# Kernel tuning notes

Measured on AMD Instinct MI355X. Metric: run time of the kernel, lower is better.

Reference implementation:

```python
import jax, jax.numpy as jnp
import numpy as np

NEG_SLOPE = 0.2  # PyG GATConv default negative_slope
EPS = 1e-16     # PyG softmax denominator epsilon


def gat_layer(x, src, dst, W, att_src, att_dst, bias, N):
    """PyG-style GATConv: gather -> leaky-relu score -> segment softmax -> scatter-add.
    x: [N, F_in], W: [F_in, H*C], att_src/att_dst: [H, C], bias: [H*C].
    src/dst: [E] edge endpoints (messages flow src -> dst), self-loops included.
    """
    H, C = att_src.shape
    h = (x @ W).reshape(N, H, C)                       # [N, H, C]
    a_s = jnp.sum(h * att_src, axis=-1)                # [N, H]
    a_d = jnp.sum(h * att_dst, axis=-1)                # [N, H]
    e = a_s[src] + a_d[dst]                            # [E, H]
    e = jnp.where(e > 0, e, NEG_SLOPE * e)             # leaky relu
    m = jax.ops.segment_max(e, dst, num_segments=N)    # [N, H] (self-loops ensure every node hit)
    p = jnp.exp(e - m[dst])                            # [E, H]
    s = jax.ops.segment_sum(p, dst, num_segments=N)    # [N, H]
    alpha = p / (s[dst] + EPS)                         # [E, H]
    out = jax.ops.segment_sum(alpha[:, :, None] * h[src], dst, num_segments=N)  # [N, H, C]
    return out.reshape(N, H * C) + bias


def setup_inputs() -> dict:
    key = jax.random.key(0)
    ks = jax.random.split(key, 12)
    N, E = 100000, 1600000
    x = jax.random.normal(ks[0], (N, 1), dtype=jnp.float32)
    edge_index = jax.random.randint(ks[1], (2, E), 0, N, dtype=jnp.int32)
    sc = 0.1
    # conv1: in=1, heads=4, out=8
    W1 = jax.random.normal(ks[2], (1, 32), dtype=jnp.float32) * sc
    att_src1 = jax.random.normal(ks[3], (4, 8), dtype=jnp.float32) * sc
    att_dst1 = jax.random.normal(ks[4], (4, 8), dtype=jnp.float32) * sc
    bias1 = jnp.zeros((32,), dtype=jnp.float32)
    # conv2: in=32, heads=8, out=8
    W2 = jax.random.normal(ks[5], (32, 64), dtype=jnp.float32) * sc
    att_src2 = jax.random.normal(ks[6], (8, 8), dtype=jnp.float32) * sc
    att_dst2 = jax.random.normal(ks[7], (8, 8), dtype=jnp.float32) * sc
    bias2 = jnp.zeros((64,), dtype=jnp.float32)
    # fc2: 64 -> 1
    fc_w = jax.random.normal(ks[8], (64, 1), dtype=jnp.float32) * sc
    fc_b = jnp.zeros((1,), dtype=jnp.float32)
    return {"x": x, "edge_index": edge_index,
            "W1": W1, "att_src1": att_src1, "att_dst1": att_dst1, "bias1": bias1,
            "W2": W2, "att_src2": att_src2, "att_dst2": att_dst2, "bias2": bias2,
            "fc_w": fc_w, "fc_b": fc_b}


def reference(x, edge_index, W1, att_src1, att_dst1, bias1,
              W2, att_src2, att_dst2, bias2, fc_w, fc_b):
    N = x.shape[0]
    loop = jnp.arange(N, dtype=edge_index.dtype)       # add_self_loops=True (PyG default)
    src = jnp.concatenate([edge_index[0], loop])
    dst = jnp.concatenate([edge_index[1], loop])
    h = jax.nn.elu(gat_layer(x, src, dst, W1, att_src1, att_dst1, bias1, N))
    h = jax.nn.elu(gat_layer(h, src, dst, W2, att_src2, att_dst2, bias2, N))
    return h @ fc_w + fc_b                             # [N, 1]
```

## Files before the change

### kernel.cpp

```cpp
#include <hip/hip_runtime.h>
#include <hip/hip_fp16.h>
#include <cmath>

#define TPB 256
#define NSLOPE 0.2f
#define SEPS 1e-16f

#define BSH 7
#define BNODES 128
#define NBMAX 1024
#define NCHUNK 512
#define SCTPB 1024
#define SCSTAGE 3360
#define STAGE 2816
#define MAXDEG 96

__device__ __forceinline__ float lrelu(float v) { return v > 0.f ? v : NSLOPE * v; }
__device__ __forceinline__ float elu1(float v)  { return v > 0.f ? v : expm1f(v); }
__device__ __forceinline__ float elu1f(float v) { return v > 0.f ? v : __expf(v) - 1.f; }

__global__ void k_prep(const float* __restrict__ W1, const float* __restrict__ as1,
                       const float* __restrict__ ad1, float* __restrict__ SD,
                       unsigned* __restrict__ bucketCursor, int NB, unsigned cap) {
    int t = threadIdx.x;
    for (int i = t; i < NB; i += blockDim.x) bucketCursor[(size_t)i * 16] = (unsigned)i * cap;
    if (t < 8) {
        int h = t & 3;
        const float* att = (t >= 4) ? ad1 : as1;
        float acc = 0.f;
        #pragma unroll
        for (int c = 0; c < 8; ++c) acc += W1[h*8+c] * att[h*8+c];
        SD[t] = acc;
    }
}

__global__ void k_bscatter(const int* __restrict__ srcI, const int* __restrict__ dstI,
                           int E, int N, int NB, int chunk,
                           unsigned* __restrict__ bucketCursor, int* __restrict__ pk) {
    __shared__ int cnt[NBMAX];
    __shared__ unsigned base[NBMAX];
    __shared__ int offl[NBMAX];
    __shared__ int rval[SCSTAGE];
    __shared__ unsigned short rbkt[SCSTAGE];
    int t = threadIdx.x;
    int ET = E + N;
    int beg = blockIdx.x * chunk;
    int end = min(beg + chunk, ET);
    int m = end - beg;
    for (int i = t; i < NBMAX; i += blockDim.x) cnt[i] = 0;
    __syncthreads();
    for (int e = beg + t; e < end; e += blockDim.x) {
        int d = (e < E) ? dstI[e] : (e - E);
        atomicAdd(&cnt[d >> BSH], 1);
    }
    __syncthreads();
    int v = (t < NBMAX) ? cnt[t] : 0;
    if (t < NBMAX) base[t] = (unsigned)v;
    __syncthreads();
    for (int off = 1; off < NBMAX; off <<= 1) {
        unsigned u = (t >= off && t < NBMAX) ? base[t - off] : 0u;
        __syncthreads();
        if (t < NBMAX) base[t] += u;
        __syncthreads();
    }
    if (t < NBMAX) offl[t] = (int)base[t] - v;
    __syncthreads();
    if (t < NB) {
        base[t] = v ? atomicAdd(&bucketCursor[(size_t)t * 16], (unsigned)v) : 0u;
        cnt[t] = 0;
    }
    __syncthreads();
    if (m <= SCSTAGE) {
        for (int e = beg + t; e < end; e += blockDim.x) {
            int s, d;
            if (e < E) { s = srcI[e]; d = dstI[e]; } else { s = d = e - E; }
            int b = d >> BSH;
            int r = atomicAdd(&cnt[b], 1);
            int slot = offl[b] + r;
            rval[slot] = (s << BSH) | (d & (BNODES - 1));
            rbkt[slot] = (unsigned short)b;
        }
        __syncthreads();
        for (int slot = t; slot < m; slot += blockDim.x) {
            int b = rbkt[slot];
            pk[base[b] + (unsigned)(slot - offl[b])] = rval[slot];
        }
    } else {
        for (int e = beg + t; e < end; e += blockDim.x) {
            int s, d;
            if (e < E) { s = srcI[e]; d = dstI[e]; } else { s = d = e - E; }
            int b = d >> BSH;
            int r = atomicAdd(&cnt[b], 1);
            pk[base[b] + (unsigned)r] = (s << BSH) | (d & (BNODES - 1));
        }
    }
}

__global__ void k_mega(const int* __restrict__ pk, const unsigned* __restrict__ bucketCursor,
                       unsigned cap,
                       const float* __restrict__ x, const float* __restrict__ SD,
                       const float* __restrict__ W1, const float* __restrict__ b1,
                       const float* __restrict__ W2, const float* __restrict__ attS,
                       const float* __restrict__ attD, int N,
                       unsigned* __restrict__ offsets, int* __restrict__ sortedSrc,
                       __half* __restrict__ h2h, float* __restrict__ aS, float* __restrict__ aD) {
    __shared__ int stage[STAGE];
    __shared__ int sorted[STAGE];
    __shared__ int cnt[BNODES];
    __shared__ int offl[BNODES];
    __shared__ float lds1[BNODES][36];
    int b = blockIdx.x, t = threadIdx.x;
    unsigned rbeg = (unsigned)b * cap;
    int m = (int)(bucketCursor[(size_t)b * 16] - rbeg);
    bool inLds = (m <= STAGE);
    if (t < BNODES) cnt[t] = 0;
    __syncthreads();
    if (inLds) {
        for (int i = t; i < m; i += TPB) stage[i] = pk[rbeg + i];
        __syncthreads();
        for (int i = t; i < m; i += TPB) atomicAdd(&cnt[stage[i] & (BNODES - 1)], 1);
    } else {
        for (int i = t; i < m; i += TPB) atomicAdd(&cnt[pk[rbeg + i] & (BNODES - 1)], 1);
    }
    __syncthreads();
    int v = (t < BNODES) ? cnt[t] : 0;
    if (t < BNODES) offl[t] = v;
    __syncthreads();
    for (int off = 1; off < BNODES; off <<= 1) {
        int u = (t >= off && t < BNODES) ? offl[t - off] : 0;
        __syncthreads();
        if (t < BNODES) offl[t] += u;
        __syncthreads();
    }
    if (t < BNODES) {
        int ex = offl[t] - v;
        int d = (b << BSH) + t;
        if (d < N) offsets[d] = ((rbeg + (unsigned)ex) << 10) | (unsigned)v;
        cnt[t] = 0;
        offl[t] = ex;
    }
    __syncthreads();
    if (inLds) {
        for (int i = t; i < m; i += TPB) {
            int p = stage[i];
            int dl = p & (BNODES - 1);
            int r = atomicAdd(&cnt[dl], 1);
            sorted[offl[dl] + r] = p >> BSH;
        }
        __syncthreads();
        for (int i = t; i < m; i += TPB) sortedSrc[rbeg + i] = sorted[i];
    } else {
        for (int i = t; i < m; i += TPB) {
            int p = pk[rbeg + i];
            int dl = p & (BNODES - 1);
            int r = atomicAdd(&cnt[dl], 1);
            sortedSrc[rbeg + (unsigned)(offl[dl] + r)] = p >> BSH;
        }
        __syncthreads();
    }
    __syncthreads();
    int n = t >> 1, half = t & 1;
    int base2 = b << BSH;
    int d2 = base2 + n;
    bool active = (d2 < N);
    float s0 = 0.f, s1 = 0.f, s2 = 0.f, s3 = 0.f;
    float g0 = 0.f, g1 = 0.f, g2 = 0.f, g3 = 0.f;
    if (active) {
        int deg = cnt[n];
        int lbeg = offl[n];
        float xd = x[d2];
        float S0 = SD[0], S1 = SD[1], S2 = SD[2], S3 = SD[3];
        float D0 = xd*SD[4], D1 = xd*SD[5], D2 = xd*SD[6], D3 = xd*SD[7];
        int dh = (deg + 1) >> 1;
        int i0 = lbeg + (half ? dh : 0);
        int rem = half ? (deg - dh) : dh;
        int i = i0;
        for (; rem >= 2; rem -= 2, i += 2) {
            int a0 = inLds ? sorted[i]   : sortedSrc[rbeg + i];
            int a1 = inLds ? sorted[i+1] : sortedSrc[rbeg + i + 1];
            float x0 = x[a0], x1 = x[a1];
            float p;
            p = __expf(lrelu(x0*S0 + D0)); s0 += p; g0 += p * x0;
            p = __expf(lrelu(x0*S1 + D1)); s1 += p; g1 += p * x0;
            p = __expf(lrelu(x0*S2 + D2)); s2 += p; g2 += p * x0;
            p = __expf(lrelu(x0*S3 + D3)); s3 += p; g3 += p * x0;
            p = __expf(lrelu(x1*S0 + D0)); s0 += p; g0 += p * x1;
            p = __expf(lrelu(x1*S1 + D1)); s1 += p; g1 += p * x1;
            p = __expf(lrelu(x1*S2 + D2)); s2 += p; g2 += p * x1;
            p = __expf(lrelu(x1*S3 + D3)); s3 += p; g3 += p * x1;
        }
        if (rem > 0) {
            int a0 = inLds ? sorted[i] : sortedSrc[rbeg + i];
            float xs = x[a0];
            float p;
            p = __expf(lrelu(xs*S0 + D0)); s0 += p; g0 += p * xs;
            p = __expf(lrelu(xs*S1 + D1)); s1 += p; g1 += p * xs;
            p = __expf(lrelu(xs*S2 + D2)); s2 += p; g2 += p * xs;
            p = __expf(lrelu(xs*S3 + D3)); s3 += p; g3 += p * xs;
        }
    }
    s0 += __shfl_xor(s0, 1); s1 += __shfl_xor(s1, 1);
    s2 += __shfl_xor(s2, 1); s3 += __shfl_xor(s3, 1);
    g0 += __shfl_xor(g0, 1); g1 += __shfl_xor(g1, 1);
    g2 += __shfl_xor(g2, 1); g3 += __shfl_xor(g3, 1);
    if (active) {
        float gg[4];
        gg[0] = g0 / (s0 + SEPS); gg[1] = g1 / (s1 + SEPS);
        gg[2] = g2 / (s2 + SEPS); gg[3] = g3 / (s3 + SEPS);
        int h0 = half * 2;
        #pragma unroll
        for (int hh = 0; hh < 2; ++hh)
            #pragma unroll
            for (int cc = 0; cc < 8; ++cc)
                lds1[n][(h0+hh)*8+cc] = elu1(gg[h0+hh] * W1[(h0+hh)*8+cc] + b1[(h0+hh)*8+cc]);
    }
    __syncthreads();
    int lane = t & 63;
    int sub = t >> 6;
    float w2r[32];
    #pragma unroll
    for (int k = 0; k < 32; ++k) w2r[k] = W2[k*64 + lane];
    float attSl = attS[lane], attDl = attD[lane];
    int nCnt = min(BNODES, N - base2);
    for (int nn = sub; nn < nCnt; nn += 4) {
        const float4* row4 = (const float4*)lds1[nn];
        float acc = 0.f;
        #pragma unroll
        for (int k4 = 0; k4 < 8; ++k4) {
            float4 rv = row4[k4];
            acc += rv.x*w2r[4*k4] + rv.y*w2r[4*k4+1] + rv.z*w2r[4*k4+2] + rv.w*w2r[4*k4+3];
        }
        int node = base2 + nn;
        h2h[(size_t)node*64 + lane] = __float2half(acc);
        float ps = acc * attSl;
        float pd = acc * attDl;
        #pragma unroll
        for (int mm = 1; mm < 8; mm <<= 1) {
            ps += __shfl_xor(ps, mm);
            pd += __shfl_xor(pd, mm);
        }
        int hh = lane >> 3, cc = lane & 7;
        if (cc == 0) aS[(size_t)node*8 + hh] = ps;
        if (cc == 1) aD[(size_t)node*8 + hh] = pd;
    }
}

__global__ void k_agg(const unsigned* __restrict__ offsets, const int* __restrict__ ss,
                      const float* __restrict__ aS, const float* __restrict__ aD,
                      const __half* __restrict__ h2h, const float* __restrict__ b2,
                      const float* __restrict__ fcw, const float* __restrict__ fcb,
                      float* __restrict__ out, int N) {
    __shared__ float pl[4][MAXDEG * 8];
    __shared__ int   sl[4][MAXDEG];
    int lane = threadIdx.x & 63;
    int w = threadIdx.x >> 6;
    int d = blockIdx.x * 4 + w;
    if (d >= N) return;
    unsigned u = offsets[d];
    unsigned beg = u >> 10;
    int deg = (int)(u & 1023u);
    int lH   = lane & 31;
    int half = lane >> 5;
    int hh   = lH >> 2;
    float sum = 0.f, ax = 0.f, ay = 0.f;
    if (deg <= MAXDEG) {
        for (int j = lane; j < deg; j += 64) sl[w][j] = ss[beg + j];
        float adp = aD[(size_t)d*8 + (lane & 7)];
        int tot = deg * 8;
        for (int base = 0; base < tot; base += 64) {
            int idx = base + lane;
            if (idx < tot) {
                int s = sl[w][idx >> 3];
                pl[w][idx] = __expf(lrelu(aS[(size_t)s*8 + (lane & 7)] + adp));
            }
        }
        int e = 0;
        for (; e + 8 <= deg; e += 8) {
            int e0 = e + half, e1 = e + 2 + half, e2 = e + 4 + half, e3 = e + 6 + half;
            int s0 = sl[w][e0], s1 = sl[w][e1], s2 = sl[w][e2], s3 = sl[w][e3];
            float p0 = pl[w][e0*8 + hh], p1 = pl[w][e1*8 + hh];
            float p2 = pl[w][e2*8 + hh], p3 = pl[w][e3*8 + hh];
            float2 g0 = __half22float2(*(const __half2*)(h2h + (size_t)s0*64 + 2*lH));
            float2 g1 = __half22float2(*(const __half2*)(h2h + (size_t)s1*64 + 2*lH));
            float2 g2 = __half22float2(*(const __half2*)(h2h + (size_t)s2*64 + 2*lH));
            float2 g3 = __half22float2(*(const __half2*)(h2h + (size_t)s3*64 + 2*lH));
            ax += p0*g0.x + p1*g1.x + p2*g2.x + p3*g3.x;
            ay += p0*g0.y + p1*g1.y + p2*g2.y + p3*g3.y;
            sum += (p0 + p1) + (p2 + p3);
        }
        for (; e + 2 <= deg; e += 2) {
            int e0 = e + half;
            int s0 = sl[w][e0];
            float p0 = pl[w][e0*8 + hh];
            float2 g0 = __half22float2(*(const __half2*)(h2h + (size_t)s0*64 + 2*lH));
            ax += p0*g0.x; ay += p0*g0.y; sum += p0;
        }
        if (e < deg) {
            int s0 = sl[w][e];
            float p0 = (half == 0) ? pl[w][e*8 + hh] : 0.f;
            float2 g0 = __half22float2(*(const __half2*)(h2h + (size_t)s0*64 + 2*lH));
            ax += p0*g0.x; ay += p0*g0.y; sum += p0;
        }
    } else {
        float adh = aD[(size_t)d*8 + hh];
        for (int e = half; e < deg; e += 2) {
            int s = ss[beg + e];
            float p = __expf(lrelu(aS[(size_t)s*8 + hh] + adh));
            float2 g = __half22float2(*(const __half2*)(h2h + (size_t)s*64 + 2*lH));
            ax += p*g.x; ay += p*g.y; sum += p;
        }
    }
    ax  += __shfl_xor(ax, 32);
    ay  += __shfl_xor(ay, 32);
    sum += __shfl_xor(sum, 32);
    float inv = 1.f / (sum + SEPS);
    float tt = elu1f(ax*inv + b2[2*lH]) * fcw[2*lH]
             + elu1f(ay*inv + b2[2*lH+1]) * fcw[2*lH+1];
    #pragma unroll
    for (int m = 16; m; m >>= 1) tt += __shfl_xor(tt, m);
    if (lane == 0) out[d] = tt + fcb[0];
}

extern "C" void kernel_launch(void* const* d_in, const int* in_sizes, int n_in,
                              void* d_out, int out_size, void* d_ws, size_t ws_size,
                              hipStream_t stream) {
    const float* x    = (const float*)d_in[0];
    const int*   ei   = (const int*)  d_in[1];
    const float* W1   = (const float*)d_in[2];
    const float* as1  = (const float*)d_in[3];
    const float* ad1  = (const float*)d_in[4];
    const float* b1   = (const float*)d_in[5];
    const float* W2   = (const float*)d_in[6];
    const float* attS2= (const float*)d_in[7];
    const float* attD2= (const float*)d_in[8];
    const float* b2   = (const float*)d_in[9];
    const float* fcw  = (const float*)d_in[10];
    const float* fcb  = (const float*)d_in[11];
    float* out = (float*)d_out;

    int N = in_sizes[0];
    int E = in_sizes[1] / 2;
    int ET = E + N;
    int NB = (N + BNODES - 1) / BNODES;
    unsigned cap = (unsigned)((ET + NB - 1) / NB + 512);
    cap = (cap + 3u) & ~3u;
    size_t padded = (size_t)NB * cap;

    const int* srcI = ei;
    const int* dstI = ei + E;

    float* ws = (float*)d_ws;
    size_t off = 0;
    float*    SD           = ws + off; off += 16;
    unsigned* bucketCursor = (unsigned*)(ws + off); off += (size_t)NBMAX * 16;
    unsigned* offsets      = (unsigned*)(ws + off); off += (size_t)N + 16;
    int*      pk           = (int*)(ws + off); off += padded;
    int*      sortedSrc    = (int*)(ws + off); off += padded;
    float*    aS2          = ws + off; off += (size_t)N * 8;
    float*    aD2          = ws + off; off += (size_t)N * 8;
    __half*   h2h          = (__half*)(ws + off); off += (size_t)N * 32;

    k_prep<<<1, 1024, 0, stream>>>(W1, as1, ad1, SD, bucketCursor, NB, cap);

    int chunk = (ET + NCHUNK - 1) / NCHUNK;
    k_bscatter<<<NCHUNK, SCTPB, 0, stream>>>(srcI, dstI, E, N, NB, chunk, bucketCursor, pk);
    k_mega    <<<NB, TPB, 0, stream>>>(pk, bucketCursor, cap, x, SD, W1, b1, W2, attS2, attD2,
                                       N, offsets, sortedSrc, h2h, aS2, aD2);
    k_agg     <<<(N + 3) / 4, TPB, 0, stream>>>(offsets, sortedSrc, aS2, aD2, h2h,
                                                b2, fcw, fcb, out, N);
}
```

Measured before the change: 229.0 us.

## Fuse all stages into one cooperative persistent kernel with grid syncs

Replaces the four separate launches (prep, bucket scatter, per-bucket sort plus layer 1, layer-2 aggregation) with one cooperative kernel of 256 blocks of 1024 threads, separated by grid.sync barriers. Bucket offsets are no longer claimed with global atomics. Per-block counts are written to a matrix and prefix-summed deterministically per bucket, and the LDS staging path of the scatter is dropped. Blocks loop over buckets and destination nodes in a persistent style, and layer 1 now uses 8 lanes per node. This aims to cut launch gaps and atomic contention, at the cost of only 256 blocks of parallelism and the overhead of the grid barriers.

Result: slower. 457.1 us (+99.6%).

```diff
diff --git a/kernel.cpp b/kernel.cpp
--- a/kernel.cpp
+++ b/kernel.cpp
@@ -1,17 +1,18 @@
 #include <hip/hip_runtime.h>
+#include <hip/hip_cooperative_groups.h>
 #include <hip/hip_fp16.h>
 #include <cmath>
 
-#define TPB 256
+namespace cg = cooperative_groups;
+
 #define NSLOPE 0.2f
 #define SEPS 1e-16f
 
 #define BSH 7
 #define BNODES 128
 #define NBMAX 1024
-#define NCHUNK 512
-#define SCTPB 1024
-#define SCSTAGE 3360
+#define NBLK 256
+#define NTHR 1024
 #define STAGE 2816
 #define MAXDEG 96
 
@@ -19,12 +20,47 @@
 __device__ __forceinline__ float elu1(float v)  { return v > 0.f ? v : expm1f(v); }
 __device__ __forceinline__ float elu1f(float v) { return v > 0.f ? v : __expf(v) - 1.f; }
 
-__global__ void k_prep(const float* __restrict__ W1, const float* __restrict__ as1,
-                       const float* __restrict__ ad1, float* __restrict__ SD,
-                       unsigned* __restrict__ bucketCursor, int NB, unsigned cap) {
-    int t = threadIdx.x;
-    for (int i = t; i < NB; i += blockDim.x) bucketCursor[(size_t)i * 16] = (unsigned)i * cap;
-    if (t < 8) {
+struct P02s { int cnt[NBMAX]; unsigned basel[NBMAX]; };
+struct P3s  { int stage[STAGE]; int sorted[STAGE]; int cnt[BNODES]; int offl[BNODES];
+              float lds1[BNODES][36]; };
+struct P4s  { float pl[16][MAXDEG * 8]; int sl[16][MAXDEG]; };
+union SmemU { P02s a; P3s b; P4s c; };
+
+__global__ __launch_bounds__(NTHR, 4)
+void k_fused(const int* __restrict__ ei, const float* __restrict__ x,
+             const float* __restrict__ W1, const float* __restrict__ as1,
+             const float* __restrict__ ad1, const float* __restrict__ b1,
+             const float* __restrict__ W2, const float* __restrict__ attS,
+             const float* __restrict__ attD, const float* __restrict__ b2,
+             const float* __restrict__ fcw, const float* __restrict__ fcb,
+             float* __restrict__ out, float* __restrict__ ws, int E, int N) {
+    __shared__ SmemU sm;
+    cg::grid_group grid = cg::this_grid();
+    int t = threadIdx.x, blk = blockIdx.x;
+    int ET = E + N;
+    int NB = (N + BNODES - 1) >> BSH;
+    unsigned cap = (unsigned)((ET + NB - 1) / NB + 512);
+    cap = (cap + 3u) & ~3u;
+    size_t padded = (size_t)NB * cap;
+
+    const int* srcI = ei;
+    const int* dstI = ei + E;
+
+    float*    SD        = ws;
+    int*      blkCnt    = (int*)(ws + 16);
+    int*      bucketLen = blkCnt + (size_t)NBMAX * NBLK;
+    unsigned* offsets   = (unsigned*)(bucketLen + NBMAX);
+    int*      pk        = (int*)(offsets + (size_t)N + 16);
+    int*      sortedSrc = pk + padded;
+    float*    aS        = (float*)(sortedSrc + padded);
+    float*    aD        = aS + (size_t)N * 8;
+    __half*   h2h       = (__half*)(aD + (size_t)N * 8);
+
+    int chunk = (ET + NBLK - 1) / NBLK;
+    int cbeg = blk * chunk;
+    int cend = min(cbeg + chunk, ET);
+
+    if (blk == 0 && t < 8) {
         int h = t & 3;
         const float* att = (t >= 4) ? ad1 : as1;
         float acc = 0.f;
@@ -32,293 +68,238 @@
         for (int c = 0; c < 8; ++c) acc += W1[h*8+c] * att[h*8+c];
         SD[t] = acc;
     }
-}
-
-__global__ void k_bscatter(const int* __restrict__ srcI, const int* __restrict__ dstI,
-                           int E, int N, int NB, int chunk,
-                           unsigned* __restrict__ bucketCursor, int* __restrict__ pk) {
-    __shared__ int cnt[NBMAX];
-    __shared__ unsigned base[NBMAX];
-    __shared__ int offl[NBMAX];
-    __shared__ int rval[SCSTAGE];
-    __shared__ unsigned short rbkt[SCSTAGE];
-    int t = threadIdx.x;
-    int ET = E + N;
-    int beg = blockIdx.x * chunk;
-    int end = min(beg + chunk, ET);
-    int m = end - beg;
-    for (int i = t; i < NBMAX; i += blockDim.x) cnt[i] = 0;
+    for (int i = t; i < NB; i += NTHR) sm.a.cnt[i] = 0;
     __syncthreads();
-    for (int e = beg + t; e < end; e += blockDim.x) {
+    for (int e = cbeg + t; e < cend; e += NTHR) {
         int d = (e < E) ? dstI[e] : (e - E);
-        atomicAdd(&cnt[d >> BSH], 1);
+        atomicAdd(&sm.a.cnt[d >> BSH], 1);
     }
     __syncthreads();
-    int v = (t < NBMAX) ? cnt[t] : 0;
-    if (t < NBMAX) base[t] = (unsigned)v;
+    for (int j = t; j < NB; j += NTHR) blkCnt[(size_t)j * NBLK + blk] = sm.a.cnt[j];
+    grid.sync();
+
+    {
+        int tid = blk * NTHR + t;
+        if (tid < NB) {
+            unsigned run = (unsigned)tid * cap;
+            size_t rowb = (size_t)tid * NBLK;
+            for (int b = 0; b < NBLK; ++b) {
+                int c = blkCnt[rowb + b];
+                blkCnt[rowb + b] = (int)run;
+                run += (unsigned)c;
+            }
+            bucketLen[tid] = (int)(run - (unsigned)tid * cap);
+        }
+    }
+    grid.sync();
+
+    for (int j = t; j < NB; j += NTHR) {
+        sm.a.basel[j] = (unsigned)blkCnt[(size_t)j * NBLK + blk];
+        sm.a.cnt[j] = 0;
+    }
     __syncthreads();
-    for (int off = 1; off < NBMAX; off <<= 1) {
-        unsigned u = (t >= off && t < NBMAX) ? base[t - off] : 0u;
-        __syncthreads();
-        if (t < NBMAX) base[t] += u;
-        __syncthreads();
-    }
-    if (t < NBMAX) offl[t] = (int)base[t] - v;
-    __syncthreads();
-    if (t < NB) {
-        base[t] = v ? atomicAdd(&bucketCursor[(size_t)t * 16], (unsigned)v) : 0u;
-        cnt[t] = 0;
-    }
-    __syncthreads();
-    if (m <= SCSTAGE) {
-        for (int e = beg + t; e < end; e += blockDim.x) {
-            int s, d;
-            if (e < E) { s = srcI[e]; d = dstI[e]; } else { s = d = e - E; }
-            int b = d >> BSH;
-            int r = atomicAdd(&cnt[b], 1);
-            int slot = offl[b] + r;
-            rval[slot] = (s << BSH) | (d & (BNODES - 1));
-            rbkt[slot] = (unsigned short)b;
-        }
-        __syncthreads();
-        for (int slot = t; slot < m; slot += blockDim.x) {
-            int b = rbkt[slot];
-            pk[base[b] + (unsigned)(slot - offl[b])] = rval[slot];
-        }
-    } else {
-        for (int e = beg + t; e < end; e += blockDim.x) {
-            int s, d;
-            if (e < E) { s = srcI[e]; d = dstI[e]; } else { s = d = e - E; }
-            int b = d >> BSH;
-            int r = atomicAdd(&cnt[b], 1);
-            pk[base[b] + (unsigned)r] = (s << BSH) | (d & (BNODES - 1));
-        }
-    }
-}
-
-__global__ void k_mega(const int* __restrict__ pk, const unsigned* __restrict__ bucketCursor,
-                       unsigned cap,
-                       const float* __restrict__ x, const float* __restrict__ SD,
-                       const float* __restrict__ W1, const float* __restrict__ b1,
-                       const float* __restrict__ W2, const float* __restrict__ attS,
-                       const float* __restrict__ attD, int N,
-                       unsigned* __restrict__ offsets, int* __restrict__ sortedSrc,
-                       __half* __restrict__ h2h, float* __restrict__ aS, float* __restrict__ aD) {
-    __shared__ int stage[STAGE];
-    __shared__ int sorted[STAGE];
-    __shared__ int cnt[BNODES];
-    __shared__ int offl[BNODES];
-    __shared__ float lds1[BNODES][36];
-    int b = blockIdx.x, t = threadIdx.x;
-    unsigned rbeg = (unsigned)b * cap;
-    int m = (int)(bucketCursor[(size_t)b * 16] - rbeg);
-    bool inLds = (m <= STAGE);
-    if (t < BNODES) cnt[t] = 0;
-    __syncthreads();
-    if (inLds) {
-        for (int i = t; i < m; i += TPB) stage[i] = pk[rbeg + i];
-        __syncthreads();
-        for (int i = t; i < m; i += TPB) atomicAdd(&cnt[stage[i] & (BNODES - 1)], 1);
-    } else {
-        for (int i = t; i < m; i += TPB) atomicAdd(&cnt[pk[rbeg + i] & (BNODES - 1)], 1);
-    }
-    __syncthreads();
-    int v = (t < BNODES) ? cnt[t] : 0;
-    if (t < BNODES) offl[t] = v;
-    __syncthreads();
-    for (int off = 1; off < BNODES; off <<= 1) {
-        int u = (t >= off && t < BNODES) ? offl[t - off] : 0;
-        __syncthreads();
-        if (t < BNODES) offl[t] += u;
-        __syncthreads();
-    }
-    if (t < BNODES) {
-        int ex = offl[t] - v;
-        int d = (b << BSH) + t;
-        if (d < N) offsets[d] = ((rbeg + (unsigned)ex) << 10) | (unsigned)v;
-        cnt[t] = 0;
-        offl[t] = ex;
-    }
-    __syncthreads();
-    if (inLds) {
-        for (int i = t; i < m; i += TPB) {
-            int p = stage[i];
-            int dl = p & (BNODES - 1);
-            int r = atomicAdd(&cnt[dl], 1);
-            sorted[offl[dl] + r] = p >> BSH;
-        }
-        __syncthreads();
-        for (int i = t; i < m; i += TPB) sortedSrc[rbeg + i] = sorted[i];
-    } else {
-        for (int i = t; i < m; i += TPB) {
-            int p = pk[rbeg + i];
-            int dl = p & (BNODES - 1);
-            int r = atomicAdd(&cnt[dl], 1);
-            sortedSrc[rbeg + (unsigned)(offl[dl] + r)] = p >> BSH;
-        }
-        __syncthreads();
-    }
-    __syncthreads();
-    int n = t >> 1, half = t & 1;
-    int base2 = b << BSH;
-    int d2 = base2 + n;
-    bool active = (d2 < N);
-    float s0 = 0.f, s1 = 0.f, s2 = 0.f, s3 = 0.f;
-    float g0 = 0.f, g1 = 0.f, g2 = 0.f, g3 = 0.f;
-    if (active) {
-        int deg = cnt[n];
-        int lbeg = offl[n];
-        float xd = x[d2];
-        float S0 = SD[0], S1 = SD[1], S2 = SD[2], S3 = SD[3];
-        float D0 = xd*SD[4], D1 = xd*SD[5], D2 = xd*SD[6], D3 = xd*SD[7];
-        int dh = (deg + 1) >> 1;
-        int i0 = lbeg + (half ? dh : 0);
-        int rem = half ? (deg - dh) : dh;
-        int i = i0;
-        for (; rem >= 2; rem -= 2, i += 2) {
-            int a0 = inLds ? sorted[i]   : sortedSrc[rbeg + i];
-            int a1 = inLds ? sorted[i+1] : sortedSrc[rbeg + i + 1];
-            float x0 = x[a0], x1 = x[a1];
-            float p;
-            p = __expf(lrelu(x0*S0 + D0)); s0 += p; g0 += p * x0;
-            p = __expf(lrelu(x0*S1 + D1)); s1 += p; g1 += p * x0;
-            p = __expf(lrelu(x0*S2 + D2)); s2 += p; g2 += p * x0;
-            p = __expf(lrelu(x0*S3 + D3)); s3 += p; g3 += p * x0;
-            p = __expf(lrelu(x1*S0 + D0)); s0 += p; g0 += p * x1;
-            p = __expf(lrelu(x1*S1 + D1)); s1 += p; g1 += p * x1;
-            p = __expf(lrelu(x1*S2 + D2)); s2 += p; g2 += p * x1;
-            p = __expf(lrelu(x1*S3 + D3)); s3 += p; g3 += p * x1;
-        }
-        if (rem > 0) {
-            int a0 = inLds ? sorted[i] : sortedSrc[rbeg + i];
-            float xs = x[a0];
-            float p;
-            p = __expf(lrelu(xs*S0 + D0)); s0 += p; g0 += p * xs;
-            p = __expf(lrelu(xs*S1 + D1)); s1 += p; g1 += p * xs;
-            p = __expf(lrelu(xs*S2 + D2)); s2 += p; g2 += p * xs;
-            p = __expf(lrelu(xs*S3 + D3)); s3 += p; g3 += p * xs;
-        }
-    }
-    s0 += __shfl_xor(s0, 1); s1 += __shfl_xor(s1, 1);
-    s2 += __shfl_xor(s2, 1); s3 += __shfl_xor(s3, 1);
-    g0 += __shfl_xor(g0, 1); g1 += __shfl_xor(g1, 1);
-    g2 += __shfl_xor(g2, 1); g3 += __shfl_xor(g3, 1);
-    if (active) {
-        float gg[4];
-        gg[0] = g0 / (s0 + SEPS); gg[1] = g1 / (s1 + SEPS);
-        gg[2] = g2 / (s2 + SEPS); gg[3] = g3 / (s3 + SEPS);
-        int h0 = half * 2;
-        #pragma unroll
-        for (int hh = 0; hh < 2; ++hh)
-            #pragma unroll
-            for (int cc = 0; cc < 8; ++cc)
-                lds1[n][(h0+hh)*8+cc] = elu1(gg[h0+hh] * W1[(h0+hh)*8+cc] + b1[(h0+hh)*8+cc]);
-    }
-    __syncthreads();
+    for (int e = cbeg + t; e < cend; e += NTHR) {
+        int s, d;
+        if (e < E) { s = srcI[e]; d = dstI[e]; } else { s = d = e - E; }
+        int j = d >> BSH;
+        int r = atomicAdd(&sm.a.cnt[j], 1);
+        pk[sm.a.basel[j] + (unsigned)r] = (s << BSH) | (d & (BNODES - 1));
+    }
+    grid.sync();
+
+    float S0 = SD[0], S1 = SD[1], S2 = SD[2], S3 = SD[3];
+    float SD4 = SD[4], SD5 = SD[5], SD6 = SD[6], SD7 = SD[7];
     int lane = t & 63;
-    int sub = t >> 6;
+    int wv = t >> 6;
     float w2r[32];
     #pragma unroll
     for (int k = 0; k < 32; ++k) w2r[k] = W2[k*64 + lane];
     float attSl = attS[lane], attDl = attD[lane];
-    int nCnt = min(BNODES, N - base2);
-    for (int nn = sub; nn < nCnt; nn += 4) {
-        const float4* row4 = (const float4*)lds1[nn];
-        float acc = 0.f;
-        #pragma unroll
-        for (int k4 = 0; k4 < 8; ++k4) {
-            float4 rv = row4[k4];
-            acc += rv.x*w2r[4*k4] + rv.y*w2r[4*k4+1] + rv.z*w2r[4*k4+2] + rv.w*w2r[4*k4+3];
-        }
-        int node = base2 + nn;
-        h2h[(size_t)node*64 + lane] = __float2half(acc);
-        float ps = acc * attSl;
-        float pd = acc * attDl;
-        #pragma unroll
-        for (int mm = 1; mm < 8; mm <<= 1) {
-            ps += __shfl_xor(ps, mm);
-            pd += __shfl_xor(pd, mm);
-        }
-        int hh = lane >> 3, cc = lane & 7;
-        if (cc == 0) aS[(size_t)node*8 + hh] = ps;
-        if (cc == 1) aD[(size_t)node*8 + hh] = pd;
-    }
-}
-
-__global__ void k_agg(const unsigned* __restrict__ offsets, const int* __restrict__ ss,
-                      const float* __restrict__ aS, const float* __restrict__ aD,
-                      const __half* __restrict__ h2h, const float* __restrict__ b2,
-                      const float* __restrict__ fcw, const float* __restrict__ fcb,
-                      float* __restrict__ out, int N) {
-    __shared__ float pl[4][MAXDEG * 8];
-    __shared__ int   sl[4][MAXDEG];
-    int lane = threadIdx.x & 63;
-    int w = threadIdx.x >> 6;
-    int d = blockIdx.x * 4 + w;
-    if (d >= N) return;
-    unsigned u = offsets[d];
-    unsigned beg = u >> 10;
-    int deg = (int)(u & 1023u);
-    int lH   = lane & 31;
-    int half = lane >> 5;
-    int hh   = lH >> 2;
-    float sum = 0.f, ax = 0.f, ay = 0.f;
-    if (deg <= MAXDEG) {
-        for (int j = lane; j < deg; j += 64) sl[w][j] = ss[beg + j];
-        float adp = aD[(size_t)d*8 + (lane & 7)];
-        int tot = deg * 8;
-        for (int base = 0; base < tot; base += 64) {
-            int idx = base + lane;
-            if (idx < tot) {
-                int s = sl[w][idx >> 3];
-                pl[w][idx] = __expf(lrelu(aS[(size_t)s*8 + (lane & 7)] + adp));
-            }
-        }
-        int e = 0;
-        for (; e + 8 <= deg; e += 8) {
-            int e0 = e + half, e1 = e + 2 + half, e2 = e + 4 + half, e3 = e + 6 + half;
-            int s0 = sl[w][e0], s1 = sl[w][e1], s2 = sl[w][e2], s3 = sl[w][e3];
-            float p0 = pl[w][e0*8 + hh], p1 = pl[w][e1*8 + hh];
-            float p2 = pl[w][e2*8 + hh], p3 = pl[w][e3*8 + hh];
-            float2 g0 = __half22float2(*(const __half2*)(h2h + (size_t)s0*64 + 2*lH));
-            float2 g1 = __half22float2(*(const __half2*)(h2h + (size_t)s1*64 + 2*lH));
-            float2 g2 = __half22float2(*(const __half2*)(h2h + (size_t)s2*64 + 2*lH));
-            float2 g3 = __half22float2(*(const __half2*)(h2h + (size_t)s3*64 + 2*lH));
-            ax += p0*g0.x + p1*g1.x + p2*g2.x + p3*g3.x;
-            ay += p0*g0.y + p1*g1.y + p2*g2.y + p3*g3.y;
-            sum += (p0 + p1) + (p2 + p3);
-        }
-        for (; e + 2 <= deg; e += 2) {
-            int e0 = e + half;
-            int s0 = sl[w][e0];
-            float p0 = pl[w][e0*8 + hh];
-            float2 g0 = __half22float2(*(const __half2*)(h2h + (size_t)s0*64 + 2*lH));
-            ax += p0*g0.x; ay += p0*g0.y; sum += p0;
-        }
-        if (e < deg) {
-            int s0 = sl[w][e];
-            float p0 = (half == 0) ? pl[w][e*8 + hh] : 0.f;
-            float2 g0 = __half22float2(*(const __half2*)(h2h + (size_t)s0*64 + 2*lH));
-            ax += p0*g0.x; ay += p0*g0.y; sum += p0;
-        }
-    } else {
-        float adh = aD[(size_t)d*8 + hh];
-        for (int e = half; e < deg; e += 2) {
-            int s = ss[beg + e];
-            float p = __expf(lrelu(aS[(size_t)s*8 + hh] + adh));
-            float2 g = __half22float2(*(const __half2*)(h2h + (size_t)s*64 + 2*lH));
-            ax += p*g.x; ay += p*g.y; sum += p;
-        }
-    }
-    ax  += __shfl_xor(ax, 32);
-    ay  += __shfl_xor(ay, 32);
-    sum += __shfl_xor(sum, 32);
-    float inv = 1.f / (sum + SEPS);
-    float tt = elu1f(ax*inv + b2[2*lH]) * fcw[2*lH]
-             + elu1f(ay*inv + b2[2*lH+1]) * fcw[2*lH+1];
-    #pragma unroll
-    for (int m = 16; m; m >>= 1) tt += __shfl_xor(tt, m);
-    if (lane == 0) out[d] = tt + fcb[0];
+    for (int b = blk; b < NB; b += NBLK) {
+        unsigned rbeg = (unsigned)b * cap;
+        int m = bucketLen[b];
+        bool inLds = (m <= STAGE);
+        __syncthreads();
+        if (t < BNODES) sm.b.cnt[t] = 0;
+        __syncthreads();
+        if (inLds) {
+            for (int i = t; i < m; i += NTHR) sm.b.stage[i] = pk[rbeg + i];
+            __syncthreads();
+            for (int i = t; i < m; i += NTHR) atomicAdd(&sm.b.cnt[sm.b.stage[i] & (BNODES-1)], 1);
+        } else {
+            for (int i = t; i < m; i += NTHR) atomicAdd(&sm.b.cnt[pk[rbeg + i] & (BNODES-1)], 1);
+        }
+        __syncthreads();
+        int v = (t < BNODES) ? sm.b.cnt[t] : 0;
+        if (t < BNODES) sm.b.offl[t] = v;
+        __syncthreads();
+        for (int off = 1; off < BNODES; off <<= 1) {
+            int u = (t >= off && t < BNODES) ? sm.b.offl[t - off] : 0;
+            __syncthreads();
+            if (t < BNODES) sm.b.offl[t] += u;
+            __syncthreads();
+        }
+        if (t < BNODES) {
+            int ex = sm.b.offl[t] - v;
+            int d = (b << BSH) + t;
+            if (d < N) offsets[d] = ((rbeg + (unsigned)ex) << 10) | (unsigned)v;
+            sm.b.cnt[t] = 0;
+            sm.b.offl[t] = ex;
+        }
+        __syncthreads();
+        if (inLds) {
+            for (int i = t; i < m; i += NTHR) {
+                int p = sm.b.stage[i];
+                int dl = p & (BNODES - 1);
+                int r = atomicAdd(&sm.b.cnt[dl], 1);
+                sm.b.sorted[sm.b.offl[dl] + r] = p >> BSH;
+            }
+            __syncthreads();
+            for (int i = t; i < m; i += NTHR) sortedSrc[rbeg + i] = sm.b.sorted[i];
+        } else {
+            for (int i = t; i < m; i += NTHR) {
+                int p = pk[rbeg + i];
+                int dl = p & (BNODES - 1);
+                int r = atomicAdd(&sm.b.cnt[dl], 1);
+                sortedSrc[rbeg + (unsigned)(sm.b.offl[dl] + r)] = p >> BSH;
+            }
+            __syncthreads();
+        }
+        __syncthreads();
+        int n = t >> 3, oct = t & 7;
+        int d2 = (b << BSH) + n;
+        bool active = (d2 < N);
+        float s0 = 0.f, s1 = 0.f, s2 = 0.f, s3 = 0.f;
+        float g0 = 0.f, g1 = 0.f, g2 = 0.f, g3 = 0.f;
+        if (active) {
+            int deg = sm.b.cnt[n];
+            int lbeg = sm.b.offl[n];
+            float xd = x[d2];
+            float D0 = xd*SD4, D1 = xd*SD5, D2 = xd*SD6, D3 = xd*SD7;
+            for (int i = lbeg + oct; i < lbeg + deg; i += 8) {
+                int a0 = inLds ? sm.b.sorted[i] : sortedSrc[rbeg + i];
+                float xs = x[a0];
+                float p;
+                p = __expf(lrelu(xs*S0 + D0)); s0 += p; g0 += p * xs;
+                p = __expf(lrelu(xs*S1 + D1)); s1 += p; g1 += p * xs;
+                p = __expf(lrelu(xs*S2 + D2)); s2 += p; g2 += p * xs;
+                p = __expf(lrelu(xs*S3 + D3)); s3 += p; g3 += p * xs;
+            }
+        }
+        s0 += __shfl_xor(s0, 1); s0 += __shfl_xor(s0, 2); s0 += __shfl_xor(s0, 4);
+        s1 += __shfl_xor(s1, 1); s1 += __shfl_xor(s1, 2); s1 += __shfl_xor(s1, 4);
+        s2 += __shfl_xor(s2, 1); s2 += __shfl_xor(s2, 2); s2 += __shfl_xor(s2, 4);
+        s3 += __shfl_xor(s3, 1); s3 += __shfl_xor(s3, 2); s3 += __shfl_xor(s3, 4);
+        g0 += __shfl_xor(g0, 1); g0 += __shfl_xor(g0, 2); g0 += __shfl_xor(g0, 4);
+        g1 += __shfl_xor(g1, 1); g1 += __shfl_xor(g1, 2); g1 += __shfl_xor(g1, 4);
+        g2 += __shfl_xor(g2, 1); g2 += __shfl_xor(g2, 2); g2 += __shfl_xor(g2, 4);
+        g3 += __shfl_xor(g3, 1); g3 += __shfl_xor(g3, 2); g3 += __shfl_xor(g3, 4);
+        if (active) {
+            int h = oct >> 1, c0 = (oct & 1) * 4;
+            float sq = (h == 0) ? s0 : (h == 1) ? s1 : (h == 2) ? s2 : s3;
+            float gq = (h == 0) ? g0 : (h == 1) ? g1 : (h == 2) ? g2 : g3;
+            float gg = gq / (sq + SEPS);
+            #pragma unroll
+            for (int cc = 0; cc < 4; ++cc)
+                sm.b.lds1[n][h*8 + c0 + cc] =
+                    elu1(gg * W1[h*8 + c0 + cc] + b1[h*8 + c0 + cc]);
+        }
+        __syncthreads();
+        int base2 = b << BSH;
+        int nCnt = min(BNODES, N - base2);
+        for (int nn = wv; nn < nCnt; nn += 16) {
+            const float4* row4 = (const float4*)sm.b.lds1[nn];
+            float acc = 0.f;
+            #pragma unroll
+            for (int k4 = 0; k4 < 8; ++k4) {
+                float4 rv = row4[k4];
+                acc += rv.x*w2r[4*k4] + rv.y*w2r[4*k4+1] + rv.z*w2r[4*k4+2] + rv.w*w2r[4*k4+3];
+            }
+            int node = base2 + nn;
+            h2h[(size_t)node*64 + lane] = __float2half(acc);
+            float ps = acc * attSl;
+            float pd = acc * attDl;
+            #pragma unroll
+            for (int mm = 1; mm < 8; mm <<= 1) {
+                ps += __shfl_xor(ps, mm);
+                pd += __shfl_xor(pd, mm);
+            }
+            int hh = lane >> 3, cc = lane & 7;
+            if (cc == 0) aS[(size_t)node*8 + hh] = ps;
+            if (cc == 1) aD[(size_t)node*8 + hh] = pd;
+        }
+    }
+    grid.sync();
+
+    {
+        float* plw = sm.c.pl[wv];
+        int*   slw = sm.c.sl[wv];
+        int lH   = lane & 31;
+        int half = lane >> 5;
+        int hh   = lH >> 2;
+        for (int d = blk * 16 + wv; d < N; d += NBLK * 16) {
+            unsigned u = offsets[d];
+            unsigned beg = u >> 10;
+            int deg = (int)(u & 1023u);
+            float sum = 0.f, ax = 0.f, ay = 0.f;
+            if (deg <= MAXDEG) {
+                for (int j = lane; j < deg; j += 64) slw[j] = sortedSrc[beg + j];
+                float adp = aD[(size_t)d*8 + (lane & 7)];
+                int tot = deg * 8;
+                for (int base = 0; base < tot; base += 64) {
+                    int idx = base + lane;
+                    if (idx < tot) {
+                        int s = slw[idx >> 3];
+                        plw[idx] = __expf(lrelu(aS[(size_t)s*8 + (lane & 7)] + adp));
+                    }
+                }
+                int e = 0;
+                for (; e + 8 <= deg; e += 8) {
+                    int e0 = e + half, e1 = e + 2 + half, e2 = e + 4 + half, e3 = e + 6 + half;
+                    int s0 = slw[e0], s1 = slw[e1], s2 = slw[e2], s3 = slw[e3];
+                    float p0 = plw[e0*8 + hh], p1 = plw[e1*8 + hh];
+                    float p2 = plw[e2*8 + hh], p3 = plw[e3*8 + hh];
+                    float2 g0 = __half22float2(*(const __half2*)(h2h + (size_t)s0*64 + 2*lH));
+                    float2 g1 = __half22float2(*(const __half2*)(h2h + (size_t)s1*64 + 2*lH));
+                    float2 g2 = __half22float2(*(const __half2*)(h2h + (size_t)s2*64 + 2*lH));
+                    float2 g3 = __half22float2(*(const __half2*)(h2h + (size_t)s3*64 + 2*lH));
+                    ax += p0*g0.x + p1*g1.x + p2*g2.x + p3*g3.x;
+                    ay += p0*g0.y + p1*g1.y + p2*g2.y + p3*g3.y;
+                    sum += (p0 + p1) + (p2 + p3);
+                }
+                for (; e + 2 <= deg; e += 2) {
+                    int e0 = e + half;
+                    int s0 = slw[e0];
+                    float p0 = plw[e0*8 + hh];
+                    float2 g0 = __half22float2(*(const __half2*)(h2h + (size_t)s0*64 + 2*lH));
+                    ax += p0*g0.x; ay += p0*g0.y; sum += p0;
+                }
+                if (e < deg) {
+                    int s0 = slw[e];
+                    float p0 = (half == 0) ? plw[e*8 + hh] : 0.f;
+                    float2 g0 = __half22float2(*(const __half2*)(h2h + (size_t)s0*64 + 2*lH));
+                    ax += p0*g0.x; ay += p0*g0.y; sum += p0;
+                }
+            } else {
+                float adh = aD[(size_t)d*8 + hh];
+                for (int e = half; e < deg; e += 2) {
+                    int s = sortedSrc[beg + e];
+                    float p = __expf(lrelu(aS[(size_t)s*8 + hh] + adh));
+                    float2 g = __half22float2(*(const __half2*)(h2h + (size_t)s*64 + 2*lH));
+                    ax += p*g.x; ay += p*g.y; sum += p;
+                }
+            }
+            ax  += __shfl_xor(ax, 32);
+            ay  += __shfl_xor(ay, 32);
+            sum += __shfl_xor(sum, 32);
+            float inv = 1.f / (sum + SEPS);
+            float tt = elu1f(ax*inv + b2[2*lH]) * fcw[2*lH]
+                     + elu1f(ay*inv + b2[2*lH+1]) * fcw[2*lH+1];
+            #pragma unroll
+            for (int mq = 16; mq; mq >>= 1) tt += __shfl_xor(tt, mq);
+            if (lane == 0) out[d] = tt + fcb[0];
+        }
+    }
 }
 
 extern "C" void kernel_launch(void* const* d_in, const int* in_sizes, int n_in,
@@ -337,35 +318,14 @@
     const float* fcw  = (const float*)d_in[10];
     const float* fcb  = (const float*)d_in[11];
     float* out = (float*)d_out;
-
+    float* ws  = (float*)d_ws;
+
+    int E = in_sizes[1] / 2;
     int N = in_sizes[0];
-    int E = in_sizes[1] / 2;
-    int ET = E + N;
-    int NB = (N + BNODES - 1) / BNODES;
-    unsigned cap = (unsigned)((ET + NB - 1) / NB + 512);
-    cap = (cap + 3u) & ~3u;
-    size_t padded = (size_t)NB * cap;
-
-    const int* srcI = ei;
-    const int* dstI = ei + E;
-
-    float* ws = (float*)d_ws;
-    size_t off = 0;
-    float*    SD           = ws + off; off += 16;
-    unsigned* bucketCursor = (unsigned*)(ws + off); off += (size_t)NBMAX * 16;
-    unsigned* offsets      = (unsigned*)(ws + off); off += (size_t)N + 16;
-    int*      pk           = (int*)(ws + off); off += padded;
-    int*      sortedSrc    = (int*)(ws + off); off += padded;
-    float*    aS2          = ws + off; off += (size_t)N * 8;
-    float*    aD2          = ws + off; off += (size_t)N * 8;
-    __half*   h2h          = (__half*)(ws + off); off += (size_t)N * 32;
-
-    k_prep<<<1, 1024, 0, stream>>>(W1, as1, ad1, SD, bucketCursor, NB, cap);
-
-    int chunk = (ET + NCHUNK - 1) / NCHUNK;
-    k_bscatter<<<NCHUNK, SCTPB, 0, stream>>>(srcI, dstI, E, N, NB, chunk, bucketCursor, pk);
-    k_mega    <<<NB, TPB, 0, stream>>>(pk, bucketCursor, cap, x, SD, W1, b1, W2, attS2, attD2,
-                                       N, offsets, sortedSrc, h2h, aS2, aD2);
-    k_agg     <<<(N + 3) / 4, TPB, 0, stream>>>(offsets, sortedSrc, aS2, aD2, h2h,
-                                                b2, fcw, fcb, out, N);
+
+    void* kargs[] = { (void*)&ei, (void*)&x, (void*)&W1, (void*)&as1, (void*)&ad1,
+                      (void*)&b1, (void*)&W2, (void*)&attS2, (void*)&attD2, (void*)&b2,
+                      (void*)&fcw, (void*)&fcb, (void*)&out, (void*)&ws,
+                      (void*)&E, (void*)&N };
+    hipLaunchCooperativeKernel((void*)k_fused, dim3(NBLK), dim3(NTHR), kargs, 0, stream);
 }
```
